# Optimization experiments

Hardware: AMD Instinct MI355X
Metric: run time of the kernel (lower is better)

## Reference

```python
import jax, jax.numpy as jnp
import numpy as np

TAU = 0.5

def setup_inputs() -> dict:
    key = jax.random.key(0)
    kx, ky = jax.random.split(key)
    B, H = 8192, 256
    x = jax.random.normal(kx, (B, H), dtype=jnp.float32)
    y = jax.random.normal(ky, (B, H), dtype=jnp.float32)
    return {"x": x, "y": y}

def reference(x, y):
    # L2-normalize rows
    x_norm = x / jnp.linalg.norm(x, axis=1, keepdims=True)
    y_norm = y / jnp.linalg.norm(y, axis=1, keepdims=True)
    xy_norm = jnp.concatenate([x_norm, y_norm], axis=0)  # [2N, H]
    yx_norm = jnp.concatenate([y_norm, x_norm], axis=0)  # [2N, H]
    # [2N, 2N] cosine-similarity matrix (dominant memory traffic)
    sim_mat_1 = xy_norm @ xy_norm.T
    exp_mat = jnp.exp(sim_mat_1 / TAU)
    exp_row_sum = jnp.sum(exp_mat, axis=1)
    exp_diag = jnp.diagonal(exp_mat)
    denominator = exp_row_sum - exp_diag
    # diag(xy_norm @ yx_norm.T) is the row-wise dot product (avoids redundant NxN matmul)
    pos_sim = jnp.sum(xy_norm * yx_norm, axis=1)
    numerator = jnp.exp(pos_sim / TAU)
    nt_xent = -jnp.log(numerator / denominator)
    return jnp.mean(nt_xent)
```

## Files before the change

kernel.cpp:

```cpp
#include <hip/hip_runtime.h>
#include <hip/hip_bf16.h>
#include <math.h>

constexpr int NROWS = 8192;
constexpr int HDIM  = 256;
constexpr int N2    = 16384;
constexpr int TM    = 256;
constexpr int BK    = 32;
constexpr int NCHUNK = HDIM / BK;
constexpr int PIECE = TM * BK;
constexpr int NTILE = N2 / TM;
constexpr int NBLK  = NTILE * (NTILE + 1) / 2;

constexpr float PRESCALE = 1.69864357f;

typedef __attribute__((ext_vector_type(4))) float floatx4;
typedef __attribute__((ext_vector_type(8))) short shortx8;

__device__ __forceinline__ void async_copy16(const void* gptr, void* lptr) {
    __builtin_amdgcn_global_load_lds(
        (const __attribute__((address_space(1))) unsigned int*)gptr,
        (__attribute__((address_space(3))) unsigned int*)lptr, 16, 0, 0);
}

#define WAIT_VM0()   __builtin_amdgcn_s_waitcnt(0x0F70)
#define MEMFENCE()   __asm__ __volatile__("" ::: "memory")
#define RAW_BARRIER() do { MEMFENCE(); __builtin_amdgcn_s_barrier(); MEMFENCE(); } while (0)

#define DPP_ROW_SHL_ADD(v, CTRL) do {                                        \
    union { float f; int i; } _u, _r; _u.f = (v);                            \
    _r.i = __builtin_amdgcn_update_dpp(0, _u.i, (CTRL), 0xF, 0xF, true);     \
    (v) += _r.f; } while (0)

__global__ __launch_bounds__(256) void normalize_kernel(
    const float* __restrict__ x, const float* __restrict__ y,
    __hip_bfloat16* __restrict__ Z, float* __restrict__ pos,
    float* __restrict__ rowsum, float* __restrict__ out)
{
    const int wave = threadIdx.x >> 6, lane = threadIdx.x & 63;
    const int row  = blockIdx.x * 4 + wave;

    const float4 xv = ((const float4*)x)[row * 64 + lane];
    const float4 yv = ((const float4*)y)[row * 64 + lane];

    float sx  = xv.x*xv.x + xv.y*xv.y + xv.z*xv.z + xv.w*xv.w;
    float sy  = yv.x*yv.x + yv.y*yv.y + yv.z*yv.z + yv.w*yv.w;
    float sxy = xv.x*yv.x + xv.y*yv.y + xv.z*yv.z + xv.w*yv.w;
    #pragma unroll
    for (int m = 1; m < 64; m <<= 1) {
        sx  += __shfl_xor(sx,  m);
        sy  += __shfl_xor(sy,  m);
        sxy += __shfl_xor(sxy, m);
    }
    const float rxn = rsqrtf(sx), ryn = rsqrtf(sy);
    const float rx = rxn * PRESCALE, ry = ryn * PRESCALE;

    union { ushort4 u; __hip_bfloat16 h[4]; } zx, zy;
    zx.h[0] = __float2bfloat16(xv.x * rx); zx.h[1] = __float2bfloat16(xv.y * rx);
    zx.h[2] = __float2bfloat16(xv.z * rx); zx.h[3] = __float2bfloat16(xv.w * rx);
    zy.h[0] = __float2bfloat16(yv.x * ry); zy.h[1] = __float2bfloat16(yv.y * ry);
    zy.h[2] = __float2bfloat16(yv.z * ry); zy.h[3] = __float2bfloat16(yv.w * ry);
    ((ushort4*)Z)[row * 64 + lane]             = zx.u;
    ((ushort4*)Z)[(row + NROWS) * 64 + lane]   = zy.u;

    if (lane == 0) {
        const float p = sxy * rxn * ryn;
        pos[row]         = p;
        pos[row + NROWS] = p;
    }
    const int gt = blockIdx.x * 256 + threadIdx.x;
    if (gt < N2) rowsum[gt] = 0.f;
    if (gt == 0) out[0] = 0.f;
}

__global__ __launch_bounds__(512, 2) void simgemm_kernel(
    const __hip_bfloat16* __restrict__ Z, float* __restrict__ rowsum)
{
    const int b = blockIdx.x;
    const int k = b & 7;
    const int m = b >> 3;
    int bi, bj;
    if (m < 36) {
        int ti = (int)((17.0f - sqrtf(289.0f - 8.0f * (float)m)) * 0.5f);
        if (m < ti * (17 - ti) / 2) ti--;
        else if (m >= (ti + 1) * (16 - ti) / 2) ti++;
        const int tj = ti + (m - ti * (17 - ti) / 2);
        bi = k * 8 + ti;
        bj = k * 8 + tj;
    } else {
        const int m2 = m - 36;
        const int hh = m2 >> 5;
        const int r  = m2 & 31;
        const int h  = hh * 8 + k;
        const int q  = h >> 1;
        const int sub = h & 1;
        int gi = 0;
        #pragma unroll
        for (int t = 6; t > 0; --t)
            if (q >= t * (15 - t) / 2) { gi = t; break; }
        const int gj = gi + 1 + (q - gi * (15 - gi) / 2);
        bi = gi * 8 + sub * 4 + (r >> 3);
        bj = gj * 8 + (r & 7);
    }
    const bool diag = (bi == bj);

    __shared__ alignas(16) __hip_bfloat16 tiles[4 * PIECE];
    __shared__ float rs[TM];
    __shared__ float cs[TM];
    __hip_bfloat16* tA = tiles;
    __hip_bfloat16* tB = tiles + PIECE;

    const int tid  = threadIdx.x;
    const int wave = tid >> 6;
    const int lane = tid & 63;
    const int wm   = wave & 1;
    const int wn   = wave >> 1;
    const int g    = lane >> 4;
    const int m15  = lane & 15;

    if (tid < TM) { rs[tid] = 0.f; cs[tid] = 0.f; }

    const int st_r0  = wave * 32 + (lane >> 2);
    const int st_c   = (lane & 3) ^ ((lane >> 3) & 3);
    const __hip_bfloat16* gA0 = Z + (size_t)(bi * TM + st_r0) * HDIM + st_c * 8;
    const __hip_bfloat16* gA1 = gA0 + 16 * HDIM;
    const __hip_bfloat16* gB0 = Z + (size_t)(bj * TM + st_r0) * HDIM + st_c * 8;
    const __hip_bfloat16* gB1 = gB0 + 16 * HDIM;
    __hip_bfloat16* lA0 = tA + (wave * 32) * BK;
    __hip_bfloat16* lA1 = tA + (wave * 32 + 16) * BK;
    __hip_bfloat16* lB0 = tB + (wave * 32) * BK;
    __hip_bfloat16* lB1 = tB + (wave * 32 + 16) * BK;

    const int sw = g ^ ((m15 >> 1) & 3);
    const __hip_bfloat16* rA = tA + (wm * 128 + m15) * BK + sw * 8;
    const __hip_bfloat16* rB = tB + (wn * 64  + m15) * BK + sw * 8;

    floatx4 acc[8][4] = {};

    #define STAGE(ck)  do {                                                  \
        const int _o = ((ck) & 1) * 2 * PIECE;                               \
        async_copy16(gA0 + (ck) * BK, lA0 + _o);                             \
        async_copy16(gA1 + (ck) * BK, lA1 + _o);                             \
        async_copy16(gB0 + (ck) * BK, lB0 + _o);                             \
        async_copy16(gB1 + (ck) * BK, lB1 + _o);                             \
    } while (0)

    STAGE(0);

    #pragma unroll
    for (int s = 0; s < NCHUNK; ++s) {
        WAIT_VM0();
        RAW_BARRIER();
        if (s + 1 < NCHUNK) STAGE(s + 1);

        const int bo = (s & 1) * 2 * PIECE;
        shortx8 af[8], bfr[4];
        #pragma unroll
        for (int f = 0; f < 8; ++f)
            af[f]  = *(const shortx8*)(rA + bo + f * 16 * BK);
        #pragma unroll
        for (int f = 0; f < 4; ++f)
            bfr[f] = *(const shortx8*)(rB + bo + f * 16 * BK);

        __builtin_amdgcn_s_setprio(1);
        #pragma unroll
        for (int fm = 0; fm < 8; ++fm)
            #pragma unroll
            for (int fn = 0; fn < 4; ++fn)
                acc[fm][fn] = __builtin_amdgcn_mfma_f32_16x16x32_bf16(
                    af[fm], bfr[fn], acc[fm][fn], 0, 0, 0);
        __builtin_amdgcn_s_setprio(0);
    }
    #undef STAGE

    float rp[8][4] = {{0.f}};
    float cp[4]    = {0.f};

    if (!diag) {
        #pragma unroll
        for (int fm = 0; fm < 8; ++fm)
            #pragma unroll
            for (int fn = 0; fn < 4; ++fn) {
                const floatx4 a = acc[fm][fn];
                #pragma unroll
                for (int q = 0; q < 4; ++q) {
                    const float e = __builtin_amdgcn_exp2f(a[q]);
                    rp[fm][q] += e;
                    cp[fn]    += e;
                }
            }
    } else {
        #pragma unroll
        for (int fm = 0; fm < 8; ++fm)
            #pragma unroll
            for (int fn = 0; fn < 4; ++fn) {
                const floatx4 a = acc[fm][fn];
                const int cl = wn * 64 + fn * 16 + m15;
                #pragma unroll
                for (int q = 0; q < 4; ++q) {
                    const int rl = wm * 128 + fm * 16 + g * 4 + q;
                    float e = __builtin_amdgcn_exp2f(a[q]);
                    if (cl <= rl) e = 0.f;
                    rp[fm][q] += e;
                    cp[fn]    += e;
                }
            }
    }

    #pragma unroll
    for (int fm = 0; fm < 8; ++fm)
        #pragma unroll
        for (int q = 0; q < 4; ++q) {
            float v = rp[fm][q];
            DPP_ROW_SHL_ADD(v, 0x101);
            DPP_ROW_SHL_ADD(v, 0x102);
            DPP_ROW_SHL_ADD(v, 0x104);
            DPP_ROW_SHL_ADD(v, 0x108);
            rp[fm][q] = v;
        }
    if (m15 == 0) {
        #pragma unroll
        for (int fm = 0; fm < 8; ++fm)
            #pragma unroll
            for (int q = 0; q < 4; ++q)
                atomicAdd(&rs[wm * 128 + fm * 16 + g * 4 + q], rp[fm][q]);
    }

    #pragma unroll
    for (int mask = 16; mask < 64; mask <<= 1)
        #pragma unroll
        for (int fn = 0; fn < 4; ++fn)
            cp[fn] += __shfl_xor(cp[fn], mask);
    if (g == 0) {
        #pragma unroll
        for (int fn = 0; fn < 4; ++fn)
            atomicAdd(&cs[wn * 64 + fn * 16 + m15], cp[fn]);
    }

    __syncthreads();
    if (tid < TM) {
        atomicAdd(&rowsum[(size_t)bi * TM + tid], rs[tid]);
        atomicAdd(&rowsum[(size_t)bj * TM + tid], cs[tid]);
    }
}

__global__ __launch_bounds__(1024) void finalize_kernel(
    const float* __restrict__ rowsum, const float* __restrict__ pos,
    float* __restrict__ out)
{
    const int i = threadIdx.x + blockIdx.x * 1024;
    float s = logf(rowsum[i]) - 2.0f * pos[i];
    #pragma unroll
    for (int off = 32; off; off >>= 1) s += __shfl_down(s, off);
    __shared__ float sh[16];
    const int lt = threadIdx.x;
    if ((lt & 63) == 0) sh[lt >> 6] = s;
    __syncthreads();
    if (lt == 0) {
        float tot = 0.f;
        #pragma unroll
        for (int w = 0; w < 16; ++w) tot += sh[w];
        atomicAdd(out, tot / (float)N2);
    }
}

extern "C" void kernel_launch(void* const* d_in, const int* in_sizes, int n_in,
                              void* d_out, int out_size, void* d_ws, size_t ws_size,
                              hipStream_t stream)
{
    const float* x = (const float*)d_in[0];
    const float* y = (const float*)d_in[1];

    __hip_bfloat16* Z = (__hip_bfloat16*)d_ws;
    float* rowsum = (float*)((char*)d_ws + (size_t)N2 * HDIM * sizeof(__hip_bfloat16));
    float* pos    = rowsum + N2;

    normalize_kernel<<<NROWS / 4, 256, 0, stream>>>(x, y, Z, pos, rowsum, (float*)d_out);
    simgemm_kernel<<<NBLK, 512, 0, stream>>>(Z, rowsum);
    finalize_kernel<<<N2 / 1024, 1024, 0, stream>>>(rowsum, pos, (float*)d_out);
}
```

Measured before the change: 159.5 us.

## Triple-buffer LDS and prefetch next-chunk MFMA fragments during compute

Moves the shared-memory staging from two buffers to three, so the global-to-LDS copy for chunk s+2 is issued while chunk s is being computed. The K loop is fully unrolled into a register-level software pipeline: the B fragments and A fragments for the next chunk are loaded from LDS in between two halves of the MFMA block, using double-buffered B registers. The aim is to hide LDS read latency and global load latency behind MFMA work. In exchange, LDS use per block grows by half and more vector registers are live, which may lower occupancy.

```diff
diff --git a/kernel.cpp b/kernel.cpp
--- a/kernel.cpp
+++ b/kernel.cpp
@@ -23,6 +23,7 @@
         (__attribute__((address_space(3))) unsigned int*)lptr, 16, 0, 0);
 }
 
+#define GATE(IMM)    __builtin_amdgcn_s_waitcnt(IMM)
 #define WAIT_VM0()   __builtin_amdgcn_s_waitcnt(0x0F70)
 #define MEMFENCE()   __asm__ __volatile__("" ::: "memory")
 #define RAW_BARRIER() do { MEMFENCE(); __builtin_amdgcn_s_barrier(); MEMFENCE(); } while (0)
@@ -104,7 +105,7 @@
     }
     const bool diag = (bi == bj);
 
-    __shared__ alignas(16) __hip_bfloat16 tiles[4 * PIECE];
+    __shared__ alignas(16) __hip_bfloat16 tiles[6 * PIECE];
     __shared__ float rs[TM];
     __shared__ float cs[TM];
     __hip_bfloat16* tA = tiles;
@@ -136,9 +137,10 @@
     const __hip_bfloat16* rB = tB + (wn * 64  + m15) * BK + sw * 8;
 
     floatx4 acc[8][4] = {};
+    shortx8 af[8], bfA[4], bfB[4];
 
     #define STAGE(ck)  do {                                                  \
-        const int _o = ((ck) & 1) * 2 * PIECE;                               \
+        const int _o = ((ck) % 3) * 2 * PIECE;                               \
         async_copy16(gA0 + (ck) * BK, lA0 + _o);                             \
         async_copy16(gA1 + (ck) * BK, lA1 + _o);                             \
         async_copy16(gB0 + (ck) * BK, lB0 + _o);                             \
@@ -146,31 +148,64 @@
     } while (0)
 
     STAGE(0);
-
-    #pragma unroll
-    for (int s = 0; s < NCHUNK; ++s) {
-        WAIT_VM0();
-        RAW_BARRIER();
-        if (s + 1 < NCHUNK) STAGE(s + 1);
-
-        const int bo = (s & 1) * 2 * PIECE;
-        shortx8 af[8], bfr[4];
-        #pragma unroll
-        for (int f = 0; f < 8; ++f)
-            af[f]  = *(const shortx8*)(rA + bo + f * 16 * BK);
-        #pragma unroll
-        for (int f = 0; f < 4; ++f)
-            bfr[f] = *(const shortx8*)(rB + bo + f * 16 * BK);
-
-        __builtin_amdgcn_s_setprio(1);
-        #pragma unroll
-        for (int fm = 0; fm < 8; ++fm)
-            #pragma unroll
-            for (int fn = 0; fn < 4; ++fn)
-                acc[fm][fn] = __builtin_amdgcn_mfma_f32_16x16x32_bf16(
-                    af[fm], bfr[fn], acc[fm][fn], 0, 0, 0);
-        __builtin_amdgcn_s_setprio(0);
-    }
+    STAGE(1);
+    GATE(0x0F74);
+    RAW_BARRIER();
+    #pragma unroll
+    for (int f = 0; f < 4; ++f)
+        bfA[f] = *(const shortx8*)(rB + f * 16 * BK);
+    #pragma unroll
+    for (int f = 0; f < 8; ++f)
+        af[f] = *(const shortx8*)(rA + f * 16 * BK);
+
+    #define BODY(S, BFC, BFN) do {                                           \
+        WAIT_VM0();          \
+        RAW_BARRIER();                  \
+        const int _bo = (((S) + 1) % 3) * 2 * PIECE;                         \
+        _Pragma("unroll")                                                    \
+        for (int f = 0; f < 4; ++f)                                          \
+            BFN[f] = *(const shortx8*)(rB + _bo + f * 16 * BK);              \
+        if ((S) + 2 < NCHUNK) STAGE((S) + 2);                                \
+        __builtin_amdgcn_s_setprio(1);                                       \
+        _Pragma("unroll")                                                    \
+        for (int fm = 0; fm < 4; ++fm)                                       \
+            _Pragma("unroll")                                                \
+            for (int fn = 0; fn < 4; ++fn)                                   \
+                acc[fm][fn] = __builtin_amdgcn_mfma_f32_16x16x32_bf16(       \
+                    af[fm], BFC[fn], acc[fm][fn], 0, 0, 0);                  \
+        __builtin_amdgcn_s_setprio(0);                                       \
+        _Pragma("unroll")                                                    \
+        for (int f = 0; f < 4; ++f)          \
+            af[f] = *(const shortx8*)(rA + _bo + f * 16 * BK);               \
+        __builtin_amdgcn_s_setprio(1);                                       \
+        _Pragma("unroll")                                                    \
+        for (int fm = 4; fm < 8; ++fm)                                       \
+            _Pragma("unroll")                                                \
+            for (int fn = 0; fn < 4; ++fn)                                   \
+                acc[fm][fn] = __builtin_amdgcn_mfma_f32_16x16x32_bf16(       \
+                    af[fm], BFC[fn], acc[fm][fn], 0, 0, 0);                  \
+        __builtin_amdgcn_s_setprio(0);                                       \
+        _Pragma("unroll")                                                    \
+        for (int f = 4; f < 8; ++f)          \
+            af[f] = *(const shortx8*)(rA + _bo + f * 16 * BK);               \
+    } while (0)
+
+    BODY(0, bfA, bfB);
+    BODY(1, bfB, bfA);
+    BODY(2, bfA, bfB);
+    BODY(3, bfB, bfA);
+    BODY(4, bfA, bfB);
+    BODY(5, bfB, bfA);
+    BODY(6, bfA, bfB);
+    __builtin_amdgcn_s_setprio(1);
+    #pragma unroll
+    for (int fm = 0; fm < 8; ++fm)
+        #pragma unroll
+        for (int fn = 0; fn < 4; ++fn)
+            acc[fm][fn] = __builtin_amdgcn_mfma_f32_16x16x32_bf16(
+                af[fm], bfB[fn], acc[fm][fn], 0, 0, 0);
+    __builtin_amdgcn_s_setprio(0);
+    #undef BODY
     #undef STAGE
 
     float rp[8][4] = {{0.f}};
```

After: 153.9 us. 3.5% less time.
